# Performance work log

Measured on AMD Instinct MI355X. Metric: run time of the kernel, lower is better.

## Reference

```python
import jax, jax.numpy as jnp
import numpy as np

B = 262144
Z_DIM = 128
H = 100


def setup_inputs() -> dict:
    key = jax.random.key(0)
    ks = jax.random.split(key, 7)
    x = jax.random.normal(ks[0], (B, Z_DIM), dtype=jnp.float32)
    # torch.nn.Linear default init ~ U(-1/sqrt(fan_in), 1/sqrt(fan_in)); use scaled normals
    w1 = jax.random.normal(ks[1], (H, Z_DIM), dtype=jnp.float32) / np.sqrt(Z_DIM)
    b1 = jax.random.normal(ks[2], (H,), dtype=jnp.float32) * 0.01
    w2 = jax.random.normal(ks[3], (H, H), dtype=jnp.float32) / np.sqrt(H)
    b2 = jax.random.normal(ks[4], (H,), dtype=jnp.float32) * 0.01
    w3 = jax.random.normal(ks[5], (9, H), dtype=jnp.float32) / np.sqrt(H)
    b3 = jax.random.normal(ks[6], (9,), dtype=jnp.float32) * 0.01
    return {"x": x, "w1": w1, "b1": b1, "w2": w2, "b2": b2, "w3": w3, "b3": b3}


def reference(x, w1, b1, w2, b2, w3, b3):
    h = jax.nn.relu(x @ w1.T + b1)            # [B, 100]
    h = jnp.tanh(h @ w2.T + b2)               # [B, 100]
    m = h @ w3.T + b3                         # [B, 9]
    M = m.reshape(-1, 3, 3)                   # [B, 3, 3]
    # torch.svd: M = U diag(S) V^T ; R_hat = U @ V^T == u @ vh (jax convention)
    u, s, vh = jnp.linalg.svd(M, full_matrices=False)
    R_hat = u @ vh                            # [B, 3, 3] nearest orthogonal (Procrustes)
    return R_hat.reshape(-1, 9)
```

## Files before the change

### kernel.cpp

```cpp
#include <hip/hip_runtime.h>
#include <math.h>

#define ZDIM 128
#define HDIM 100

__global__ void prep_transpose(const float* __restrict__ w1,
                               const float* __restrict__ w3,
                               float* __restrict__ w1t,
                               float* __restrict__ w3t) {
    int idx = blockIdx.x * blockDim.x + threadIdx.x;
    if (idx < HDIM * ZDIM) {
        int j = idx / ZDIM;
        int k = idx - j * ZDIM;
        w1t[k * HDIM + j] = w1[idx];
    }
    if (idx < 9 * HDIM) {
        int r = idx / HDIM;
        int i = idx - r * HDIM;
        w3t[i * 9 + r] = w3[idx];
    }
}

template<bool TR>
__global__ __launch_bounds__(256) void pose_main(
    const float* __restrict__ x,
    const float* __restrict__ w1,
    const float* __restrict__ b1,
    const float* __restrict__ w2,
    const float* __restrict__ b2,
    const float* __restrict__ w3,
    const float* __restrict__ b3,
    const float* __restrict__ w1t,
    const float* __restrict__ w3t,
    float* __restrict__ out,
    int nB)
{
    int tid = blockIdx.x * blockDim.x + threadIdx.x;
    if (tid >= nB) return;

    const float4* xrow = reinterpret_cast<const float4*>(x + (size_t)tid * ZDIM);

    float h1[HDIM];
    #pragma unroll
    for (int j = 0; j < HDIM; ++j) h1[j] = b1[j];

    #pragma unroll 1
    for (int k4 = 0; k4 < ZDIM / 4; ++k4) {
        const float4 xk = xrow[k4];
        #pragma unroll
        for (int j = 0; j < HDIM; ++j) {
            float wa, wb, wc, wd;
            if (TR) {
                const float* base = w1t + (size_t)(k4 * 4) * HDIM + j;
                wa = base[0 * HDIM];
                wb = base[1 * HDIM];
                wc = base[2 * HDIM];
                wd = base[3 * HDIM];
            } else {
                const float* base = w1 + (size_t)j * ZDIM + k4 * 4;
                wa = base[0]; wb = base[1]; wc = base[2]; wd = base[3];
            }
            float acc = h1[j];
            acc = fmaf(xk.x, wa, acc);
            acc = fmaf(xk.y, wb, acc);
            acc = fmaf(xk.z, wc, acc);
            acc = fmaf(xk.w, wd, acc);
            h1[j] = acc;
        }
    }

    #pragma unroll
    for (int j = 0; j < HDIM; ++j) h1[j] = fmaxf(h1[j], 0.0f);

    float mr[9];
    #pragma unroll
    for (int r = 0; r < 9; ++r) mr[r] = b3[r];

    #pragma unroll 1
    for (int i = 0; i < HDIM; ++i) {
        const float* w2row = w2 + (size_t)i * HDIM;
        float a0 = 0.f, a1 = 0.f, a2 = 0.f, a3 = 0.f;
        #pragma unroll
        for (int j = 0; j < HDIM; j += 4) {
            a0 = fmaf(w2row[j + 0], h1[j + 0], a0);
            a1 = fmaf(w2row[j + 1], h1[j + 1], a1);
            a2 = fmaf(w2row[j + 2], h1[j + 2], a2);
            a3 = fmaf(w2row[j + 3], h1[j + 3], a3);
        }
        float t = tanhf((a0 + a1) + (a2 + a3) + b2[i]);
        #pragma unroll
        for (int r = 0; r < 9; ++r) {
            float wv = TR ? w3t[i * 9 + r] : w3[r * HDIM + i];
            mr[r] = fmaf(wv, t, mr[r]);
        }
    }

    double X00 = mr[0], X01 = mr[1], X02 = mr[2];
    double X10 = mr[3], X11 = mr[4], X12 = mr[5];
    double X20 = mr[6], X21 = mr[7], X22 = mr[8];

    #pragma unroll 1
    for (int it = 0; it < 12; ++it) {
        double C00 = X11 * X22 - X12 * X21;
        double C01 = X12 * X20 - X10 * X22;
        double C02 = X10 * X21 - X11 * X20;
        double C10 = X02 * X21 - X01 * X22;
        double C11 = X00 * X22 - X02 * X20;
        double C12 = X01 * X20 - X00 * X21;
        double C20 = X01 * X12 - X02 * X11;
        double C21 = X02 * X10 - X00 * X12;
        double C22 = X00 * X11 - X01 * X10;
        double det = X00 * C00 + X01 * C01 + X02 * C02;
        double adet = fabs(det);
        adet = adet < 1e-300 ? 1e-300 : adet;
        double sdet = (det < 0.0) ? -adet : adet;
        double nf2 = X00*X00 + X01*X01 + X02*X02
                   + X10*X10 + X11*X11 + X12*X12
                   + X20*X20 + X21*X21 + X22*X22;
        double nc2 = C00*C00 + C01*C01 + C02*C02
                   + C10*C10 + C11*C11 + C12*C12
                   + C20*C20 + C21*C21 + C22*C22;
        double g = sqrt(sqrt(nc2 / nf2) / adet);
        double a = 0.5 * g;
        double b = 0.5 / (g * sdet);
        X00 = a * X00 + b * C00;  X01 = a * X01 + b * C01;  X02 = a * X02 + b * C02;
        X10 = a * X10 + b * C10;  X11 = a * X11 + b * C11;  X12 = a * X12 + b * C12;
        X20 = a * X20 + b * C20;  X21 = a * X21 + b * C21;  X22 = a * X22 + b * C22;
    }

    float* o = out + (size_t)tid * 9;
    o[0] = (float)X00; o[1] = (float)X01; o[2] = (float)X02;
    o[3] = (float)X10; o[4] = (float)X11; o[5] = (float)X12;
    o[6] = (float)X20; o[7] = (float)X21; o[8] = (float)X22;
}

extern "C" void kernel_launch(void* const* d_in, const int* in_sizes, int n_in,
                              void* d_out, int out_size, void* d_ws, size_t ws_size,
                              hipStream_t stream) {
    const float* x  = (const float*)d_in[0];
    const float* w1 = (const float*)d_in[1];
    const float* b1 = (const float*)d_in[2];
    const float* w2 = (const float*)d_in[3];
    const float* b2 = (const float*)d_in[4];
    const float* w3 = (const float*)d_in[5];
    const float* b3 = (const float*)d_in[6];
    float* out = (float*)d_out;

    int nB = in_sizes[0] / ZDIM;

    const size_t need = (size_t)(HDIM * ZDIM + HDIM * 9) * sizeof(float);
    float* w1t = (float*)d_ws;
    float* w3t = w1t + HDIM * ZDIM;

    dim3 block(256);
    dim3 grid((nB + 255) / 256);

    if (ws_size >= need) {
        dim3 pgrid((HDIM * ZDIM + 255) / 256);
        prep_transpose<<<pgrid, block, 0, stream>>>(w1, w3, w1t, w3t);
        pose_main<true><<<grid, block, 0, stream>>>(x, w1, b1, w2, b2, w3, b3,
                                                    w1t, w3t, out, nB);
    } else {
        pose_main<false><<<grid, block, 0, stream>>>(x, w1, b1, w2, b2, w3, b3,
                                                     nullptr, nullptr, out, nB);
    }
}
```

Measured before the change: 254.0 us.

## Block layer-1 over hidden units, add fast tanh, cut polar iterations, raise occupancy

Layer 1 is restructured to accumulate 50 hidden units at a time, looping over k in chunks of eight inputs, and the launch bounds now request 4 blocks per SIMD to lower register pressure and raise occupancy. tanhf is replaced by an exp plus reciprocal approximation. The Newton polar iteration count for the Procrustes rotation drops from 12 to 10. Together these aim to cut per-thread register use and ALU work. The trade-offs are reading x twice (once per hidden-unit half), possible spills under the tighter register bound, and some accuracy loss from the approximate tanh and fewer iterations.

```diff
diff --git a/kernel.cpp b/kernel.cpp
--- a/kernel.cpp
+++ b/kernel.cpp
@@ -3,6 +3,7 @@
 
 #define ZDIM 128
 #define HDIM 100
+#define JB   50
 
 __global__ void prep_transpose(const float* __restrict__ w1,
                                const float* __restrict__ w3,
@@ -21,8 +22,18 @@
     }
 }
 
+__device__ __forceinline__ float fast_tanh(float v) {
+    float e = __expf(2.0f * v);
+#if __has_builtin(__builtin_amdgcn_rcpf)
+    float r = __builtin_amdgcn_rcpf(e + 1.0f);
+    return (e - 1.0f) * r;
+#else
+    return (e - 1.0f) / (e + 1.0f);
+#endif
+}
+
 template<bool TR>
-__global__ __launch_bounds__(256) void pose_main(
+__global__ __launch_bounds__(256, 4) void pose_main(
     const float* __restrict__ x,
     const float* __restrict__ w1,
     const float* __restrict__ b1,
@@ -38,39 +49,41 @@
     int tid = blockIdx.x * blockDim.x + threadIdx.x;
     if (tid >= nB) return;
 
-    const float4* xrow = reinterpret_cast<const float4*>(x + (size_t)tid * ZDIM);
+    const float4* xrow4 = reinterpret_cast<const float4*>(x + (size_t)tid * ZDIM);
 
     float h1[HDIM];
-    #pragma unroll
-    for (int j = 0; j < HDIM; ++j) h1[j] = b1[j];
-
-    #pragma unroll 1
-    for (int k4 = 0; k4 < ZDIM / 4; ++k4) {
-        const float4 xk = xrow[k4];
-        #pragma unroll
-        for (int j = 0; j < HDIM; ++j) {
-            float wa, wb, wc, wd;
-            if (TR) {
-                const float* base = w1t + (size_t)(k4 * 4) * HDIM + j;
-                wa = base[0 * HDIM];
-                wb = base[1 * HDIM];
-                wc = base[2 * HDIM];
-                wd = base[3 * HDIM];
-            } else {
-                const float* base = w1 + (size_t)j * ZDIM + k4 * 4;
-                wa = base[0]; wb = base[1]; wc = base[2]; wd = base[3];
-            }
-            float acc = h1[j];
-            acc = fmaf(xk.x, wa, acc);
-            acc = fmaf(xk.y, wb, acc);
-            acc = fmaf(xk.z, wc, acc);
-            acc = fmaf(xk.w, wd, acc);
-            h1[j] = acc;
-        }
-    }
 
     #pragma unroll
-    for (int j = 0; j < HDIM; ++j) h1[j] = fmaxf(h1[j], 0.0f);
+    for (int jb = 0; jb < HDIM / JB; ++jb) {
+        float acc[JB];
+        #pragma unroll
+        for (int j = 0; j < JB; ++j) acc[j] = b1[jb * JB + j];
+
+        #pragma unroll 1
+        for (int k8 = 0; k8 < ZDIM / 8; ++k8) {
+            const float4 xa = xrow4[2 * k8 + 0];
+            const float4 xb = xrow4[2 * k8 + 1];
+            const float xs[8] = { xa.x, xa.y, xa.z, xa.w,
+                                  xb.x, xb.y, xb.z, xb.w };
+            #pragma unroll
+            for (int kk = 0; kk < 8; ++kk) {
+                const int k = k8 * 8 + kk;
+                const float xv = xs[kk];
+                if (TR) {
+                    const float* wrow = w1t + (size_t)k * HDIM + jb * JB;
+                    #pragma unroll
+                    for (int j = 0; j < JB; ++j)
+                        acc[j] = fmaf(xv, wrow[j], acc[j]);
+                } else {
+                    #pragma unroll
+                    for (int j = 0; j < JB; ++j)
+                        acc[j] = fmaf(xv, w1[(size_t)(jb * JB + j) * ZDIM + k], acc[j]);
+                }
+            }
+        }
+        #pragma unroll
+        for (int j = 0; j < JB; ++j) h1[jb * JB + j] = fmaxf(acc[j], 0.0f);
+    }
 
     float mr[9];
     #pragma unroll
@@ -87,7 +100,7 @@
             a2 = fmaf(w2row[j + 2], h1[j + 2], a2);
             a3 = fmaf(w2row[j + 3], h1[j + 3], a3);
         }
-        float t = tanhf((a0 + a1) + (a2 + a3) + b2[i]);
+        float t = fast_tanh((a0 + a1) + (a2 + a3) + b2[i]);
         #pragma unroll
         for (int r = 0; r < 9; ++r) {
             float wv = TR ? w3t[i * 9 + r] : w3[r * HDIM + i];
@@ -100,7 +113,7 @@
     double X20 = mr[6], X21 = mr[7], X22 = mr[8];
 
     #pragma unroll 1
-    for (int it = 0; it < 12; ++it) {
+    for (int it = 0; it < 10; ++it) {
         double C00 = X11 * X22 - X12 * X21;
         double C01 = X12 * X20 - X10 * X22;
         double C02 = X10 * X21 - X11 * X20;
```

New measurement: 213.1 us. -16.1%, faster.
